# Performance work log

Hardware: AMD Instinct MI355X
Metric: run time of the kernel (lower is better)

Reference implementation:

```python
import jax, jax.numpy as jnp
import numpy as np

N = 50000   # nodes
E = 800000  # edges (avg in-degree 16)
H = 4       # attention heads
F = 64      # in/out feats per head
NEG_SLOPE = 0.2  # DGL GATConv default


def setup_inputs() -> dict:
    key = jax.random.key(0)
    ks = jax.random.split(key, 12)
    s = 0.1
    x = jax.random.normal(ks[0], (N, F), jnp.float32)
    src = jax.random.randint(ks[1], (E,), 0, N, jnp.int32)
    dst = jax.random.randint(ks[2], (E,), 0, N, jnp.int32)
    W1 = (jax.random.normal(ks[3], (F, H * F), jnp.float32) * s)
    al1 = (jax.random.normal(ks[4], (H, F), jnp.float32) * s)
    ar1 = (jax.random.normal(ks[5], (H, F), jnp.float32) * s)
    b1 = jnp.zeros((H, F), jnp.float32)
    W2 = (jax.random.normal(ks[6], (F, H * F), jnp.float32) * s)
    al2 = (jax.random.normal(ks[7], (H, F), jnp.float32) * s)
    ar2 = (jax.random.normal(ks[8], (H, F), jnp.float32) * s)
    b2 = jnp.zeros((H, F), jnp.float32)
    return dict(x=x, src=src, dst=dst, W1=W1, al1=al1, ar1=ar1, b1=b1,
                W2=W2, al2=al2, ar2=ar2, b2=b2)


def _gat_layer(x, src, dst, W, al, ar, b):
    # Linear projection, split into heads: [N, H, F]
    h = (x @ W).reshape(N, H, F)
    # Per-node attention logits: [N, H]
    el = jnp.einsum('nhf,hf->nh', h, al)
    er = jnp.einsum('nhf,hf->nh', h, ar)
    # Per-edge score, LeakyReLU: [E, H]
    e = jax.nn.leaky_relu(el[src] + er[dst], NEG_SLOPE)
    # Edge-softmax over incoming edges of each dst node (segment softmax)
    emax = jax.ops.segment_max(e, dst, num_segments=N)        # [N, H]
    ee = jnp.exp(e - emax[dst])                               # [E, H]
    denom = jax.ops.segment_sum(ee, dst, num_segments=N)      # [N, H]
    alpha = ee / denom[dst]                                   # [E, H]
    # Weighted aggregation: gather src feats, scale, scatter-add to dst
    m = h[src] * alpha[..., None]                              # [E, H, F]
    out = jax.ops.segment_sum(m, dst, num_segments=N)          # [N, H, F]
    return out + b[None]


def reference(x, src, dst, W1, al1, ar1, b1, W2, al2, ar2, b2):
    # Layer 1: GATConv with tanh activation, then head-mean
    h = _gat_layer(x, src, dst, W1, al1, ar1, b1)
    h = jnp.tanh(h).mean(axis=-2)              # [N, F]
    # Layer 2: GATConv (no activation), then head-mean
    h = _gat_layer(h, src, dst, W2, al2, ar2, b2)
    return h.mean(axis=-2)                     # [N, F]
```

## Files before the change

kernel.cpp:

```cpp
#include <hip/hip_runtime.h>
#include <cfloat>
#include <cstddef>

#define NODES 50000
#define EDGES 800000
#define HEADS 4
#define FEAT  64
#define HF    256
#define NEG_SLOPE 0.2f


__global__ void zero_deg_kernel(int* __restrict__ deg) {
  int i = blockIdx.x * blockDim.x + threadIdx.x;
  if (i < NODES) deg[i] = 0;
}

__global__ void count_deg_kernel(const int* __restrict__ dst, int* __restrict__ deg) {
  int e = blockIdx.x * blockDim.x + threadIdx.x;
  if (e < EDGES) atomicAdd(&deg[dst[e]], 1);
}

__global__ __launch_bounds__(1024) void scan_kernel(const int* __restrict__ deg,
                                                    int* __restrict__ rowstart,
                                                    int* __restrict__ cursor) {
  __shared__ int wtot[16], wexcl[16];
  __shared__ int carry_s;
  const int tid = threadIdx.x, lane = tid & 63, wv = tid >> 6;
  if (tid == 0) carry_s = 0;
  __syncthreads();
  for (int base = 0; base < NODES; base += 4096) {
    const int i0 = base + tid * 4;
    int v0 = (i0 + 0 < NODES) ? deg[i0 + 0] : 0;
    int v1 = (i0 + 1 < NODES) ? deg[i0 + 1] : 0;
    int v2 = (i0 + 2 < NODES) ? deg[i0 + 2] : 0;
    int v3 = (i0 + 3 < NODES) ? deg[i0 + 3] : 0;
    const int t = v0 + v1 + v2 + v3;
    int x = t;
#pragma unroll
    for (int off = 1; off < 64; off <<= 1) {
      int u = __shfl_up(x, off, 64);
      if (lane >= off) x += u;
    }
    if (lane == 63) wtot[wv] = x;
    __syncthreads();
    if (wv == 0) {
      int wval = (lane < 16) ? wtot[lane] : 0;
      int wx = wval;
#pragma unroll
      for (int off = 1; off < 16; off <<= 1) {
        int u = __shfl_up(wx, off, 64);
        if (lane >= off) wx += u;
      }
      if (lane < 16) wexcl[lane] = wx - wval;
    }
    __syncthreads();
    const int carry = carry_s;
    int e = carry + wexcl[wv] + (x - t);
    if (i0 + 0 < NODES) { rowstart[i0 + 0] = e; cursor[i0 + 0] = e; } e += v0;
    if (i0 + 1 < NODES) { rowstart[i0 + 1] = e; cursor[i0 + 1] = e; } e += v1;
    if (i0 + 2 < NODES) { rowstart[i0 + 2] = e; cursor[i0 + 2] = e; } e += v2;
    if (i0 + 3 < NODES) { rowstart[i0 + 3] = e; cursor[i0 + 3] = e; }
    __syncthreads();
    if (tid == 1023) carry_s = carry + wexcl[15] + wtot[15];
    __syncthreads();
  }
}

__global__ void scatter_kernel(const int* __restrict__ src, const int* __restrict__ dst,
                               int* __restrict__ cursor, int* __restrict__ csr_src) {
  int e = blockIdx.x * blockDim.x + threadIdx.x;
  if (e < EDGES) {
    int pos = atomicAdd(&cursor[dst[e]], 1);
    csr_src[pos] = src[e];
  }
}

template<int ROWS>
__global__ __launch_bounds__(256) void proj_kernel(
    const float* __restrict__ x, const float* __restrict__ W,
    const float* __restrict__ al, const float* __restrict__ ar,
    float* __restrict__ h, float* __restrict__ el, float* __restrict__ er) {
  __shared__ float xs[ROWS * FEAT];
  const int c = threadIdx.x;
  const int head = c >> 6, f = c & 63;

  float Wc[FEAT];
#pragma unroll
  for (int k = 0; k < FEAT; ++k) Wc[k] = W[k * HF + c];
  const float alv = al[head * FEAT + f];
  const float arv = ar[head * FEAT + f];

  const int row0 = blockIdx.x * ROWS;
  for (int i = c; i < ROWS * FEAT; i += 256) {
    int r = row0 + (i >> 6);
    xs[i] = (r < NODES) ? x[r * FEAT + (i & 63)] : 0.f;
  }
  __syncthreads();

  for (int r = 0; r < ROWS; ++r) {
    const int row = row0 + r;
    if (row >= NODES) break;
    const float4* xr = (const float4*)&xs[r * FEAT];
    float v = 0.f;
#pragma unroll
    for (int k4 = 0; k4 < 16; ++k4) {
      float4 xv = xr[k4];
      v += xv.x * Wc[4 * k4 + 0] + xv.y * Wc[4 * k4 + 1] +
           xv.z * Wc[4 * k4 + 2] + xv.w * Wc[4 * k4 + 3];
    }
    h[(size_t)row * HF + c] = v;
    float sl = v * alv, sr = v * arv;
#pragma unroll
    for (int m = 32; m; m >>= 1) {
      sl += __shfl_xor(sl, m, 64);
      sr += __shfl_xor(sr, m, 64);
    }
    if (f == 0) {
      el[row * HEADS + head] = sl;
      er[row * HEADS + head] = sr;
    }
  }
}

__device__ __forceinline__ float lrelu(float s) { return s > 0.f ? s : NEG_SLOPE * s; }

template<int DO_TANH>
__global__ __launch_bounds__(256) void node_kernel(
    const int* __restrict__ rowstart, const int* __restrict__ deg,
    const int* __restrict__ csr_src,
    const float* __restrict__ el, const float* __restrict__ er,
    const float* __restrict__ h, const float* __restrict__ bias,
    float* __restrict__ out) {
  const int node = (blockIdx.x * blockDim.x + threadIdx.x) >> 6;
  if (node >= NODES) return;
  const int lane = threadIdx.x & 63;
  const int hh = lane >> 4, fq = lane & 15;
  const int rs = rowstart[node];
  const int dg = deg[node];

  float4 acc = make_float4(0.f, 0.f, 0.f, 0.f);

  if (dg > 0) {
    const float4 erv = *(const float4*)&er[node * 4];
    float m0 = -FLT_MAX, m1 = -FLT_MAX, m2 = -FLT_MAX, m3 = -FLT_MAX;
    for (int i = lane; i < dg; i += 64) {
      int s = csr_src[rs + i];
      float4 ev = *(const float4*)&el[s * 4];
      m0 = fmaxf(m0, lrelu(ev.x + erv.x));
      m1 = fmaxf(m1, lrelu(ev.y + erv.y));
      m2 = fmaxf(m2, lrelu(ev.z + erv.z));
      m3 = fmaxf(m3, lrelu(ev.w + erv.w));
    }
#pragma unroll
    for (int off = 32; off; off >>= 1) {
      m0 = fmaxf(m0, __shfl_xor(m0, off, 64));
      m1 = fmaxf(m1, __shfl_xor(m1, off, 64));
      m2 = fmaxf(m2, __shfl_xor(m2, off, 64));
      m3 = fmaxf(m3, __shfl_xor(m3, off, 64));
    }
    float q0 = 0.f, q1 = 0.f, q2 = 0.f, q3 = 0.f;
    for (int i = lane; i < dg; i += 64) {
      int s = csr_src[rs + i];
      float4 ev = *(const float4*)&el[s * 4];
      q0 += __expf(lrelu(ev.x + erv.x) - m0);
      q1 += __expf(lrelu(ev.y + erv.y) - m1);
      q2 += __expf(lrelu(ev.z + erv.z) - m2);
      q3 += __expf(lrelu(ev.w + erv.w) - m3);
    }
#pragma unroll
    for (int off = 32; off; off >>= 1) {
      q0 += __shfl_xor(q0, off, 64);
      q1 += __shfl_xor(q1, off, 64);
      q2 += __shfl_xor(q2, off, 64);
      q3 += __shfl_xor(q3, off, 64);
    }
    const float r0 = 1.f / q0, r1 = 1.f / q1, r2 = 1.f / q2, r3 = 1.f / q3;
    for (int base = 0; base < dg; base += 64) {
      const int cnt = min(64, dg - base);
      int sL = 0;
      float A0 = 0.f, A1 = 0.f, A2 = 0.f, A3 = 0.f;
      if (base + lane < dg) {
        sL = csr_src[rs + base + lane];
        float4 ev = *(const float4*)&el[sL * 4];
        A0 = __expf(lrelu(ev.x + erv.x) - m0) * r0;
        A1 = __expf(lrelu(ev.y + erv.y) - m1) * r1;
        A2 = __expf(lrelu(ev.z + erv.z) - m2) * r2;
        A3 = __expf(lrelu(ev.w + erv.w) - m3) * r3;
      }
      for (int i = 0; i < cnt; ++i) {
        const int s = __shfl(sL, i, 64);
        const float a0 = __shfl(A0, i, 64);
        const float a1 = __shfl(A1, i, 64);
        const float a2 = __shfl(A2, i, 64);
        const float a3 = __shfl(A3, i, 64);
        const float av = (hh == 0) ? a0 : (hh == 1) ? a1 : (hh == 2) ? a2 : a3;
        const float4 hv = *(const float4*)&h[(size_t)s * HF + hh * FEAT + fq * 4];
        acc.x += hv.x * av;
        acc.y += hv.y * av;
        acc.z += hv.z * av;
        acc.w += hv.w * av;
      }
    }
  }

  const float4 bv = *(const float4*)&bias[hh * FEAT + fq * 4];
  float vx = acc.x + bv.x, vy = acc.y + bv.y, vz = acc.z + bv.z, vw = acc.w + bv.w;
  if (DO_TANH) { vx = tanhf(vx); vy = tanhf(vy); vz = tanhf(vz); vw = tanhf(vw); }
#pragma unroll
  for (int off = 16; off <= 32; off <<= 1) {
    vx += __shfl_xor(vx, off, 64);
    vy += __shfl_xor(vy, off, 64);
    vz += __shfl_xor(vz, off, 64);
    vw += __shfl_xor(vw, off, 64);
  }
  if (hh == 0) {
    *(float4*)&out[(size_t)node * FEAT + fq * 4] =
        make_float4(vx * 0.25f, vy * 0.25f, vz * 0.25f, vw * 0.25f);
  }
}


extern "C" void kernel_launch(void* const* d_in, const int* in_sizes, int n_in,
                              void* d_out, int out_size, void* d_ws, size_t ws_size,
                              hipStream_t stream) {
  const float* x   = (const float*)d_in[0];
  const int*   src = (const int*)d_in[1];
  const int*   dst = (const int*)d_in[2];
  const float* Ws[2]  = {(const float*)d_in[3], (const float*)d_in[7]};
  const float* als[2] = {(const float*)d_in[4], (const float*)d_in[8]};
  const float* ars[2] = {(const float*)d_in[5], (const float*)d_in[9]};
  const float* bs[2]  = {(const float*)d_in[6], (const float*)d_in[10]};

  float* ws = (float*)d_ws;
  const size_t NHF = (size_t)NODES * HF;
  const size_t NF  = (size_t)NODES * FEAT;
  const size_t NH  = (size_t)NODES * HEADS;
  float* hbuf = ws;
  float* x2   = ws + NHF;
  float* el   = ws + NHF + NF;
  float* er   = el + NH;
  int* ibase   = (int*)(er + NH);
  int* deg      = ibase;
  int* rowstart = ibase + NODES;
  int* cursor   = ibase + 2 * NODES;
  int* csr_src  = ibase + 3 * NODES;
  float* outp = (float*)d_out;

  const int ROWS = 32;
  const int proj_grid = (NODES + ROWS - 1) / ROWS;
  const int edge_grid = (EDGES + 255) / 256;
  const int node_grid = (NODES * 64) / 256;
  const int n_grid    = (NODES + 255) / 256;

  zero_deg_kernel<<<n_grid, 256, 0, stream>>>(deg);
  count_deg_kernel<<<edge_grid, 256, 0, stream>>>(dst, deg);
  scan_kernel<<<1, 1024, 0, stream>>>(deg, rowstart, cursor);
  scatter_kernel<<<edge_grid, 256, 0, stream>>>(src, dst, cursor, csr_src);

  proj_kernel<ROWS><<<proj_grid, 256, 0, stream>>>(x, Ws[0], als[0], ars[0], hbuf, el, er);
  node_kernel<1><<<node_grid, 256, 0, stream>>>(rowstart, deg, csr_src, el, er,
                                                hbuf, bs[0], x2);
  proj_kernel<ROWS><<<proj_grid, 256, 0, stream>>>(x2, Ws[1], als[1], ars[1], hbuf, el, er);
  node_kernel<0><<<node_grid, 256, 0, stream>>>(rowstart, deg, csr_src, el, er,
                                                hbuf, bs[1], outp);
}
```

Measured before the change: 549.0 us.

## Store projected features in fp16 and add single-pass softmax for low-degree nodes

The projection output h is now written as half precision and converted back to fp32 inside the aggregation gather, halving the bytes moved in the dominant random-gather traffic. The node kernel also gains a fast path for nodes with degree at most 64: each lane loads its edge once and keeps scores in registers, replacing the three passes over csr_src/el. The cost is reduced precision of h (about 3 decimal digits), which may affect accuracy tolerance.

```diff
diff --git a/kernel.cpp b/kernel.cpp
--- a/kernel.cpp
+++ b/kernel.cpp
@@ -1,4 +1,5 @@
 #include <hip/hip_runtime.h>
+#include <hip/hip_fp16.h>
 #include <cfloat>
 #include <cstddef>
 
@@ -79,7 +80,7 @@
 __global__ __launch_bounds__(256) void proj_kernel(
     const float* __restrict__ x, const float* __restrict__ W,
     const float* __restrict__ al, const float* __restrict__ ar,
-    float* __restrict__ h, float* __restrict__ el, float* __restrict__ er) {
+    __half* __restrict__ h, float* __restrict__ el, float* __restrict__ er) {
   __shared__ float xs[ROWS * FEAT];
   const int c = threadIdx.x;
   const int head = c >> 6, f = c & 63;
@@ -108,7 +109,7 @@
       v += xv.x * Wc[4 * k4 + 0] + xv.y * Wc[4 * k4 + 1] +
            xv.z * Wc[4 * k4 + 2] + xv.w * Wc[4 * k4 + 3];
     }
-    h[(size_t)row * HF + c] = v;
+    h[(size_t)row * HF + c] = __float2half(v);
     float sl = v * alv, sr = v * arv;
 #pragma unroll
     for (int m = 32; m; m >>= 1) {
@@ -123,13 +124,25 @@
 }
 
 __device__ __forceinline__ float lrelu(float s) { return s > 0.f ? s : NEG_SLOPE * s; }
+
+__device__ __forceinline__ void gather_fma(const __half* __restrict__ h, int s,
+                                           int hh, int fq, float av, float4& acc) {
+  union { uint2 u; __half2 h2[2]; } cvt;
+  cvt.u = *(const uint2*)(h + (size_t)s * HF + hh * FEAT + fq * 4);
+  float2 f01 = __half22float2(cvt.h2[0]);
+  float2 f23 = __half22float2(cvt.h2[1]);
+  acc.x += f01.x * av;
+  acc.y += f01.y * av;
+  acc.z += f23.x * av;
+  acc.w += f23.y * av;
+}
 
 template<int DO_TANH>
 __global__ __launch_bounds__(256) void node_kernel(
     const int* __restrict__ rowstart, const int* __restrict__ deg,
     const int* __restrict__ csr_src,
     const float* __restrict__ el, const float* __restrict__ er,
-    const float* __restrict__ h, const float* __restrict__ bias,
+    const __half* __restrict__ h, const float* __restrict__ bias,
     float* __restrict__ out) {
   const int node = (blockIdx.x * blockDim.x + threadIdx.x) >> 6;
   if (node >= NODES) return;
@@ -142,63 +155,105 @@
 
   if (dg > 0) {
     const float4 erv = *(const float4*)&er[node * 4];
-    float m0 = -FLT_MAX, m1 = -FLT_MAX, m2 = -FLT_MAX, m3 = -FLT_MAX;
-    for (int i = lane; i < dg; i += 64) {
-      int s = csr_src[rs + i];
-      float4 ev = *(const float4*)&el[s * 4];
-      m0 = fmaxf(m0, lrelu(ev.x + erv.x));
-      m1 = fmaxf(m1, lrelu(ev.y + erv.y));
-      m2 = fmaxf(m2, lrelu(ev.z + erv.z));
-      m3 = fmaxf(m3, lrelu(ev.w + erv.w));
-    }
-#pragma unroll
-    for (int off = 32; off; off >>= 1) {
-      m0 = fmaxf(m0, __shfl_xor(m0, off, 64));
-      m1 = fmaxf(m1, __shfl_xor(m1, off, 64));
-      m2 = fmaxf(m2, __shfl_xor(m2, off, 64));
-      m3 = fmaxf(m3, __shfl_xor(m3, off, 64));
-    }
-    float q0 = 0.f, q1 = 0.f, q2 = 0.f, q3 = 0.f;
-    for (int i = lane; i < dg; i += 64) {
-      int s = csr_src[rs + i];
-      float4 ev = *(const float4*)&el[s * 4];
-      q0 += __expf(lrelu(ev.x + erv.x) - m0);
-      q1 += __expf(lrelu(ev.y + erv.y) - m1);
-      q2 += __expf(lrelu(ev.z + erv.z) - m2);
-      q3 += __expf(lrelu(ev.w + erv.w) - m3);
-    }
-#pragma unroll
-    for (int off = 32; off; off >>= 1) {
-      q0 += __shfl_xor(q0, off, 64);
-      q1 += __shfl_xor(q1, off, 64);
-      q2 += __shfl_xor(q2, off, 64);
-      q3 += __shfl_xor(q3, off, 64);
-    }
-    const float r0 = 1.f / q0, r1 = 1.f / q1, r2 = 1.f / q2, r3 = 1.f / q3;
-    for (int base = 0; base < dg; base += 64) {
-      const int cnt = min(64, dg - base);
+    if (dg <= 64) {
       int sL = 0;
-      float A0 = 0.f, A1 = 0.f, A2 = 0.f, A3 = 0.f;
-      if (base + lane < dg) {
-        sL = csr_src[rs + base + lane];
+      float s0 = -FLT_MAX, s1 = -FLT_MAX, s2 = -FLT_MAX, s3 = -FLT_MAX;
+      if (lane < dg) {
+        sL = csr_src[rs + lane];
         float4 ev = *(const float4*)&el[sL * 4];
-        A0 = __expf(lrelu(ev.x + erv.x) - m0) * r0;
-        A1 = __expf(lrelu(ev.y + erv.y) - m1) * r1;
-        A2 = __expf(lrelu(ev.z + erv.z) - m2) * r2;
-        A3 = __expf(lrelu(ev.w + erv.w) - m3) * r3;
-      }
-      for (int i = 0; i < cnt; ++i) {
+        s0 = lrelu(ev.x + erv.x);
+        s1 = lrelu(ev.y + erv.y);
+        s2 = lrelu(ev.z + erv.z);
+        s3 = lrelu(ev.w + erv.w);
+      }
+      float m0 = s0, m1 = s1, m2 = s2, m3 = s3;
+#pragma unroll
+      for (int off = 32; off; off >>= 1) {
+        m0 = fmaxf(m0, __shfl_xor(m0, off, 64));
+        m1 = fmaxf(m1, __shfl_xor(m1, off, 64));
+        m2 = fmaxf(m2, __shfl_xor(m2, off, 64));
+        m3 = fmaxf(m3, __shfl_xor(m3, off, 64));
+      }
+      float E0 = 0.f, E1 = 0.f, E2 = 0.f, E3 = 0.f;
+      if (lane < dg) {
+        E0 = __expf(s0 - m0);
+        E1 = __expf(s1 - m1);
+        E2 = __expf(s2 - m2);
+        E3 = __expf(s3 - m3);
+      }
+      float q0 = E0, q1 = E1, q2 = E2, q3 = E3;
+#pragma unroll
+      for (int off = 32; off; off >>= 1) {
+        q0 += __shfl_xor(q0, off, 64);
+        q1 += __shfl_xor(q1, off, 64);
+        q2 += __shfl_xor(q2, off, 64);
+        q3 += __shfl_xor(q3, off, 64);
+      }
+      const float A0 = E0 / q0, A1 = E1 / q1, A2 = E2 / q2, A3 = E3 / q3;
+      for (int i = 0; i < dg; ++i) {
         const int s = __shfl(sL, i, 64);
         const float a0 = __shfl(A0, i, 64);
         const float a1 = __shfl(A1, i, 64);
         const float a2 = __shfl(A2, i, 64);
         const float a3 = __shfl(A3, i, 64);
         const float av = (hh == 0) ? a0 : (hh == 1) ? a1 : (hh == 2) ? a2 : a3;
-        const float4 hv = *(const float4*)&h[(size_t)s * HF + hh * FEAT + fq * 4];
-        acc.x += hv.x * av;
-        acc.y += hv.y * av;
-        acc.z += hv.z * av;
-        acc.w += hv.w * av;
+        gather_fma(h, s, hh, fq, av, acc);
+      }
+    } else {
+      float m0 = -FLT_MAX, m1 = -FLT_MAX, m2 = -FLT_MAX, m3 = -FLT_MAX;
+      for (int i = lane; i < dg; i += 64) {
+        int s = csr_src[rs + i];
+        float4 ev = *(const float4*)&el[s * 4];
+        m0 = fmaxf(m0, lrelu(ev.x + erv.x));
+        m1 = fmaxf(m1, lrelu(ev.y + erv.y));
+        m2 = fmaxf(m2, lrelu(ev.z + erv.z));
+        m3 = fmaxf(m3, lrelu(ev.w + erv.w));
+      }
+#pragma unroll
+      for (int off = 32; off; off >>= 1) {
+        m0 = fmaxf(m0, __shfl_xor(m0, off, 64));
+        m1 = fmaxf(m1, __shfl_xor(m1, off, 64));
+        m2 = fmaxf(m2, __shfl_xor(m2, off, 64));
+        m3 = fmaxf(m3, __shfl_xor(m3, off, 64));
+      }
+      float q0 = 0.f, q1 = 0.f, q2 = 0.f, q3 = 0.f;
+      for (int i = lane; i < dg; i += 64) {
+        int s = csr_src[rs + i];
+        float4 ev = *(const float4*)&el[s * 4];
+        q0 += __expf(lrelu(ev.x + erv.x) - m0);
+        q1 += __expf(lrelu(ev.y + erv.y) - m1);
+        q2 += __expf(lrelu(ev.z + erv.z) - m2);
+        q3 += __expf(lrelu(ev.w + erv.w) - m3);
+      }
+#pragma unroll
+      for (int off = 32; off; off >>= 1) {
+        q0 += __shfl_xor(q0, off, 64);
+        q1 += __shfl_xor(q1, off, 64);
+        q2 += __shfl_xor(q2, off, 64);
+        q3 += __shfl_xor(q3, off, 64);
+      }
+      const float r0 = 1.f / q0, r1 = 1.f / q1, r2 = 1.f / q2, r3 = 1.f / q3;
+      for (int base = 0; base < dg; base += 64) {
+        const int cnt = min(64, dg - base);
+        int sL = 0;
+        float A0 = 0.f, A1 = 0.f, A2 = 0.f, A3 = 0.f;
+        if (base + lane < dg) {
+          sL = csr_src[rs + base + lane];
+          float4 ev = *(const float4*)&el[sL * 4];
+          A0 = __expf(lrelu(ev.x + erv.x) - m0) * r0;
+          A1 = __expf(lrelu(ev.y + erv.y) - m1) * r1;
+          A2 = __expf(lrelu(ev.z + erv.z) - m2) * r2;
+          A3 = __expf(lrelu(ev.w + erv.w) - m3) * r3;
+        }
+        for (int i = 0; i < cnt; ++i) {
+          const int s = __shfl(sL, i, 64);
+          const float a0 = __shfl(A0, i, 64);
+          const float a1 = __shfl(A1, i, 64);
+          const float a2 = __shfl(A2, i, 64);
+          const float a3 = __shfl(A3, i, 64);
+          const float av = (hh == 0) ? a0 : (hh == 1) ? a1 : (hh == 2) ? a2 : a3;
+          gather_fma(h, s, hh, fq, av, acc);
+        }
       }
     }
   }
@@ -235,9 +290,9 @@
   const size_t NHF = (size_t)NODES * HF;
   const size_t NF  = (size_t)NODES * FEAT;
   const size_t NH  = (size_t)NODES * HEADS;
-  float* hbuf = ws;
-  float* x2   = ws + NHF;
-  float* el   = ws + NHF + NF;
+  __half* hbuf = (__half*)ws;
+  float* x2   = ws + NHF / 2;
+  float* el   = x2 + NF;
   float* er   = el + NH;
   int* ibase   = (int*)(er + NH);
   int* deg      = ibase;
```

Result: faster. 492.3 us (-10.3%).
